# Performance work log

Measured on AMD Instinct MI355X. Metric: run time of the kernel, lower is better.

The kernel has to match this reference:

```python
import jax, jax.numpy as jnp
import numpy as np

N_NODES = 50000
N_EDGES = 800000
IN_CH = 128
OUT_CH = 64
SELF_LOOP_W = 2.0  # improved=True in GCNConv


def setup_inputs() -> dict:
    key = jax.random.key(0)
    k1, k2, k3, k4 = jax.random.split(key, 4)
    x = jax.random.normal(k1, (N_NODES, IN_CH), dtype=jnp.float32)
    edge_index = jax.random.randint(k2, (2, N_EDGES), 0, N_NODES, dtype=jnp.int64)
    edge_weight = jax.random.uniform(k3, (N_EDGES,), dtype=jnp.float32)
    W = jax.random.normal(k4, (IN_CH, OUT_CH), dtype=jnp.float32) / np.sqrt(IN_CH)
    b = jnp.zeros((OUT_CH,), dtype=jnp.float32)
    return {"x": x, "edge_index": edge_index, "edge_weight": edge_weight, "W": W, "b": b}


def reference(x, edge_index, edge_weight, W, b):
    # Only the first GCNConv layer runs (the torch loop returns after k=0).
    N = x.shape[0]
    row, col = edge_index[0], edge_index[1]  # source, target

    # gcn_norm with add_self_loops=True, improved=True (fill value 2.0)
    loop_idx = jnp.arange(N, dtype=edge_index.dtype)
    row_f = jnp.concatenate([row, loop_idx])
    col_f = jnp.concatenate([col, loop_idx])
    ew_f = jnp.concatenate([edge_weight, jnp.full((N,), SELF_LOOP_W, dtype=edge_weight.dtype)])

    deg = jax.ops.segment_sum(ew_f, col_f, num_segments=N)          # [N]
    dinv = jnp.where(deg > 0, jax.lax.rsqrt(deg), 0.0)
    norm = dinv[row_f] * ew_f * dinv[col_f]                          # [E+N]

    # linear transform then normalized sparse aggregation
    xw = x @ W                                                       # [N, out]
    msg = norm[:, None] * xw[row_f]                                  # [E+N, out] gather
    out = jax.ops.segment_sum(msg, col_f, num_segments=N)           # [N, out] scatter-add
    return out + b
```

## Files before the change

### kernel.cpp

```cpp
#include <hip/hip_runtime.h>

constexpr int N    = 50000;
constexpr int E    = 800000;
constexpr int CIN  = 128;
constexpr int COUT = 64;
constexpr float SELF_LOOP_W = 2.0f;

constexpr int NB   = (N + 63) / 64;
constexpr int CAP  = 1536;
constexpr int EPB  = 2048;
constexpr int PBLK = (E + EPB - 1) / EPB;

typedef float          vfloat4  __attribute__((ext_vector_type(4)));
typedef int            vint2    __attribute__((ext_vector_type(2)));
typedef int            vint4    __attribute__((ext_vector_type(4)));
typedef unsigned short vushort4 __attribute__((ext_vector_type(4)));

__device__ __forceinline__ unsigned short f2bf(float f) {
    unsigned int u = __float_as_uint(f);
    u += 0x7FFFu + ((u >> 16) & 1u);
    return (unsigned short)(u >> 16);
}
__device__ __forceinline__ float bf2f(unsigned short h) {
    return __uint_as_float(((unsigned int)h) << 16);
}

__global__ __launch_bounds__(512) void partition_kernel(const int* __restrict__ row,
                                                        const int* __restrict__ col,
                                                        const float* __restrict__ ew,
                                                        int* __restrict__ bcur,
                                                        float* __restrict__ deg,
                                                        vint2* __restrict__ pk) {
    __shared__ int lhist[NB];
    __shared__ int lbase[NB];
    const int t  = threadIdx.x;
    const int e  = blockIdx.x * EPB + t * 4;
    const bool valid = (e < E);

    for (int i = t; i < NB; i += 512) lhist[i] = 0;
    __syncthreads();

    vint4   c4;
    vfloat4 w4;
    if (valid) {
        c4 = *(const vint4*)(col + e);
        w4 = *(const vfloat4*)(ew + e);
        #pragma unroll
        for (int u = 0; u < 4; ++u) {
            atomicAdd(&lhist[c4[u] >> 6], 1);
            atomicAdd(&deg[c4[u]], w4[u]);
        }
    }
    __syncthreads();

    for (int i = t; i < NB; i += 512) {
        int h = lhist[i];
        if (h > 0) lbase[i] = i * CAP + atomicAdd(&bcur[i], h);
    }
    __syncthreads();

    if (valid) {
        vint4 r4 = *(const vint4*)(row + e);
        #pragma unroll
        for (int u = 0; u < 4; ++u) {
            int c   = c4[u];
            int bkt = c >> 6;
            int p   = atomicAdd(&lbase[bkt], 1);
            if (p < (bkt + 1) * CAP) {
                vint2 v;
                v.x = r4[u] | ((c & 63) << 20);
                v.y = __float_as_int(w4[u]);
                pk[p] = v;
            }
        }
    }
}

__global__ __launch_bounds__(256) void xw_kernel(const float* __restrict__ x,
                                                 const float* __restrict__ W,
                                                 const float* __restrict__ deg,
                                                 unsigned short* __restrict__ xwh,
                                                 float* __restrict__ dinv) {
    __shared__ __align__(16) float xs[64][132];

    const int t    = threadIdx.x;
    const int b    = blockIdx.x;
    const int base = b * 64;

    #pragma unroll
    for (int i = 0; i < 8; ++i) {
        int f4  = i * 256 + t;
        int r   = f4 >> 5;
        int c4  = f4 & 31;
        int node = base + r;
        if (node >= N) node = N - 1;
        *(vfloat4*)&xs[r][c4 * 4] = *(const vfloat4*)(x + (size_t)node * CIN + c4 * 4);
    }
    __syncthreads();

    if (t < 64) {
        int node = base + t;
        if (node < N) dinv[node] = rsqrtf(SELF_LOOP_W + deg[node]);
    }

    const int tc = t & 15;
    const int tn = t >> 4;

    float acc[4][4];
    #pragma unroll
    for (int i = 0; i < 4; ++i)
        #pragma unroll
        for (int j = 0; j < 4; ++j) acc[i][j] = 0.f;

    const float* Wp = W + tc * 4;
    #pragma unroll 4
    for (int k = 0; k < CIN; k += 4) {
        vfloat4 b0 = *(const vfloat4*)(Wp + (size_t)(k + 0) * COUT);
        vfloat4 b1 = *(const vfloat4*)(Wp + (size_t)(k + 1) * COUT);
        vfloat4 b2 = *(const vfloat4*)(Wp + (size_t)(k + 2) * COUT);
        vfloat4 b3 = *(const vfloat4*)(Wp + (size_t)(k + 3) * COUT);
        #pragma unroll
        for (int i = 0; i < 4; ++i) {
            vfloat4 a = *(const vfloat4*)&xs[tn * 4 + i][k];
            #pragma unroll
            for (int j = 0; j < 4; ++j)
                acc[i][j] += a[0] * b0[j] + a[1] * b1[j] + a[2] * b2[j] + a[3] * b3[j];
        }
    }

    #pragma unroll
    for (int i = 0; i < 4; ++i) {
        int node = base + tn * 4 + i;
        if (node >= N) continue;
        vushort4 hv;
        #pragma unroll
        for (int j = 0; j < 4; ++j) hv[j] = f2bf(acc[i][j]);
        *(vushort4*)(xwh + (size_t)node * COUT + tc * 4) = hv;
    }
}

__global__ __launch_bounds__(512) void aggregate_kernel(const int* __restrict__ bcur,
                                                        const vint2* __restrict__ pk,
                                                        const float* __restrict__ dinv,
                                                        const unsigned short* __restrict__ xwh,
                                                        const float* __restrict__ bias,
                                                        float* __restrict__ out) {
    __shared__ int   rawx[CAP];
    __shared__ float rawn[CAP];
    __shared__ int   s_r[CAP];
    __shared__ float s_n[CAP];
    __shared__ int   lhist[64], lofs[64], lcur[64];

    const int t    = threadIdx.x;
    const int lane = t & 63;
    const int wv   = t >> 6;
    const int b    = blockIdx.x;
    const int base = b * CAP;
    const int cnt  = min(bcur[b], CAP);

    if (t < 64) lhist[t] = 0;
    __syncthreads();

    for (int j = t; j < cnt; j += 512) {
        vint2 v = pk[base + j];
        rawx[j] = v.x;
        rawn[j] = __int_as_float(v.y) * dinv[v.x & 0xFFFFF];
        atomicAdd(&lhist[(v.x >> 20) & 63], 1);
    }
    __syncthreads();

    if (t < 64) {
        int v = lhist[t];
        int s = v;
        #pragma unroll
        for (int d = 1; d < 64; d <<= 1) {
            int u = __shfl_up(s, d);
            if (lane >= d) s += u;
        }
        lofs[t] = s - v;
        lcur[t] = s - v;
    }
    __syncthreads();

    for (int j = t; j < cnt; j += 512) {
        int xv = rawx[j];
        int p  = atomicAdd(&lcur[(xv >> 20) & 63], 1);
        s_r[p] = xv & 0xFFFFF;
        s_n[p] = rawn[j];
    }
    __syncthreads();

    const int q  = lane >> 4;
    const int c4 = lane & 15;

    for (int nd = wv; nd < 64; nd += 8) {
        int node = b * 64 + nd;
        if (node >= N) continue;
        int s0 = lofs[nd];
        int e0 = s0 + lhist[nd];

        float a0 = 0.f, a1 = 0.f, a2 = 0.f, a3 = 0.f;
        for (int i = s0; i < e0; i += 16) {
            int rr[4]; float nn[4]; vushort4 vv[4];
            #pragma unroll
            for (int u = 0; u < 4; ++u) {
                int j = i + 4 * u + q;
                bool ok = (j < e0);
                rr[u] = ok ? s_r[j] : s_r[s0];
                nn[u] = ok ? s_n[j] : 0.f;
            }
            #pragma unroll
            for (int u = 0; u < 4; ++u)
                vv[u] = *(const vushort4*)(xwh + (size_t)rr[u] * COUT + c4 * 4);
            #pragma unroll
            for (int u = 0; u < 4; ++u) {
                a0 += nn[u] * bf2f(vv[u][0]);
                a1 += nn[u] * bf2f(vv[u][1]);
                a2 += nn[u] * bf2f(vv[u][2]);
                a3 += nn[u] * bf2f(vv[u][3]);
            }
        }
        a0 += __shfl_xor(a0, 16); a0 += __shfl_xor(a0, 32);
        a1 += __shfl_xor(a1, 16); a1 += __shfl_xor(a1, 32);
        a2 += __shfl_xor(a2, 16); a2 += __shfl_xor(a2, 32);
        a3 += __shfl_xor(a3, 16); a3 += __shfl_xor(a3, 32);

        if (q == 0) {
            float dc = dinv[node];
            float s2 = SELF_LOOP_W * dc * dc;
            vushort4 sh = *(const vushort4*)(xwh + (size_t)node * COUT + c4 * 4);
            vfloat4  bv = *(const vfloat4*)(bias + c4 * 4);
            vfloat4  o;
            o[0] = dc * a0 + s2 * bf2f(sh[0]) + bv[0];
            o[1] = dc * a1 + s2 * bf2f(sh[1]) + bv[1];
            o[2] = dc * a2 + s2 * bf2f(sh[2]) + bv[2];
            o[3] = dc * a3 + s2 * bf2f(sh[3]) + bv[3];
            *(vfloat4*)(out + (size_t)node * COUT + c4 * 4) = o;
        }
    }
}

extern "C" void kernel_launch(void* const* d_in, const int* in_sizes, int n_in,
                              void* d_out, int out_size, void* d_ws, size_t ws_size,
                              hipStream_t stream) {
    const float* x  = (const float*)d_in[0];
    const int*   ei = (const int*)d_in[1];
    const float* ew = (const float*)d_in[2];
    const float* W  = (const float*)d_in[3];
    const float* b  = (const float*)d_in[4];
    float* out = (float*)d_out;

    unsigned short* xwh  = (unsigned short*)d_ws;
    float*          dinv = (float*)(xwh + (size_t)N * COUT);
    float*          deg  = dinv + N;
    int*            bcur = (int*)(deg + N);
    vint2*          pk   = (vint2*)(bcur + NB + 2);

    const int* rowp = ei;
    const int* colp = ei + E;

    hipMemsetAsync(deg, 0, (size_t)(N + NB + 2) * sizeof(int), stream);
    partition_kernel<<<PBLK, 512, 0, stream>>>(rowp, colp, ew, bcur, deg, pk);
    xw_kernel       <<<NB, 256, 0, stream>>>(x, W, deg, xwh, dinv);
    aggregate_kernel<<<NB, 512, 0, stream>>>(bcur, pk, dinv, xwh, b, out);
}
```

Baseline: 180.2 us.

## Replace block-local histogram partitioning with per-edge global atomics on sub-buckets

The partition kernel drops its shared-memory histogram, the two block barriers and the per-block base reservation. Each edge now claims a slot directly with a global atomic on one of four sub-bucket counters per destination bucket, chosen by thread index to spread contention. The aggregate kernel gathers the four sub-buckets into a contiguous shared buffer. This trades barrier and shared-atomic overhead for roughly 800K global atomics on the counters. It also caps each sub-bucket at 384 entries, so a skewed split across sub-buckets can overflow one and drop edges.

```diff
diff --git a/kernel.cpp b/kernel.cpp
--- a/kernel.cpp
+++ b/kernel.cpp
@@ -6,10 +6,10 @@
 constexpr int COUT = 64;
 constexpr float SELF_LOOP_W = 2.0f;
 
-constexpr int NB   = (N + 63) / 64;
-constexpr int CAP  = 1536;
-constexpr int EPB  = 2048;
-constexpr int PBLK = (E + EPB - 1) / EPB;
+constexpr int NB     = (N + 63) / 64;
+constexpr int SUBCAP = 384;
+constexpr int CAP    = 4 * SUBCAP;
+constexpr int PBLK   = (E + 1023) / 1024;
 
 typedef float          vfloat4  __attribute__((ext_vector_type(4)));
 typedef int            vint2    __attribute__((ext_vector_type(2)));
@@ -25,54 +25,33 @@
     return __uint_as_float(((unsigned int)h) << 16);
 }
 
-__global__ __launch_bounds__(512) void partition_kernel(const int* __restrict__ row,
+__global__ __launch_bounds__(256) void partition_kernel(const int* __restrict__ row,
                                                         const int* __restrict__ col,
                                                         const float* __restrict__ ew,
                                                         int* __restrict__ bcur,
                                                         float* __restrict__ deg,
                                                         vint2* __restrict__ pk) {
-    __shared__ int lhist[NB];
-    __shared__ int lbase[NB];
-    const int t  = threadIdx.x;
-    const int e  = blockIdx.x * EPB + t * 4;
-    const bool valid = (e < E);
-
-    for (int i = t; i < NB; i += 512) lhist[i] = 0;
-    __syncthreads();
-
-    vint4   c4;
-    vfloat4 w4;
-    if (valid) {
-        c4 = *(const vint4*)(col + e);
-        w4 = *(const vfloat4*)(ew + e);
-        #pragma unroll
-        for (int u = 0; u < 4; ++u) {
-            atomicAdd(&lhist[c4[u] >> 6], 1);
-            atomicAdd(&deg[c4[u]], w4[u]);
-        }
-    }
-    __syncthreads();
-
-    for (int i = t; i < NB; i += 512) {
-        int h = lhist[i];
-        if (h > 0) lbase[i] = i * CAP + atomicAdd(&bcur[i], h);
-    }
-    __syncthreads();
-
-    if (valid) {
-        vint4 r4 = *(const vint4*)(row + e);
-        #pragma unroll
-        for (int u = 0; u < 4; ++u) {
-            int c   = c4[u];
-            int bkt = c >> 6;
-            int p   = atomicAdd(&lbase[bkt], 1);
-            if (p < (bkt + 1) * CAP) {
-                vint2 v;
-                v.x = r4[u] | ((c & 63) << 20);
-                v.y = __float_as_int(w4[u]);
-                pk[p] = v;
-            }
-        }
+    const int t = blockIdx.x * 256 + threadIdx.x;
+    const int e = t * 4;
+    if (e >= E) return;
+
+    vint4   c4 = *(const vint4*)(col + e);
+    vint4   r4 = *(const vint4*)(row + e);
+    vfloat4 w4 = *(const vfloat4*)(ew + e);
+
+    #pragma unroll
+    for (int u = 0; u < 4; ++u) {
+        int c   = c4[u];
+        int bkt = c >> 6;
+        int sub = (threadIdx.x + u) & 3;
+        int p   = atomicAdd(&bcur[bkt * 4 + sub], 1);
+        if (p < SUBCAP) {
+            vint2 v;
+            v.x = r4[u] | ((c & 63) << 20);
+            v.y = __float_as_int(w4[u]);
+            pk[(size_t)bkt * CAP + sub * SUBCAP + p] = v;
+        }
+        atomicAdd(&deg[c], w4[u]);
     }
 }
 
@@ -155,18 +134,24 @@
     const int lane = t & 63;
     const int wv   = t >> 6;
     const int b    = blockIdx.x;
-    const int base = b * CAP;
-    const int cnt  = min(bcur[b], CAP);
+    const size_t base = (size_t)b * CAP;
 
     if (t < 64) lhist[t] = 0;
     __syncthreads();
 
-    for (int j = t; j < cnt; j += 512) {
-        vint2 v = pk[base + j];
-        rawx[j] = v.x;
-        rawn[j] = __int_as_float(v.y) * dinv[v.x & 0xFFFFF];
-        atomicAdd(&lhist[(v.x >> 20) & 63], 1);
-    }
+    int ofs = 0;
+    #pragma unroll
+    for (int s = 0; s < 4; ++s) {
+        int cs = min(bcur[b * 4 + s], SUBCAP);
+        for (int j = t; j < cs; j += 512) {
+            vint2 v = pk[base + s * SUBCAP + j];
+            rawx[ofs + j] = v.x;
+            rawn[ofs + j] = __int_as_float(v.y) * dinv[v.x & 0xFFFFF];
+            atomicAdd(&lhist[(v.x >> 20) & 63], 1);
+        }
+        ofs += cs;
+    }
+    const int cnt = ofs;
     __syncthreads();
 
     if (t < 64) {
@@ -254,13 +239,13 @@
     float*          dinv = (float*)(xwh + (size_t)N * COUT);
     float*          deg  = dinv + N;
     int*            bcur = (int*)(deg + N);
-    vint2*          pk   = (vint2*)(bcur + NB + 2);
+    vint2*          pk   = (vint2*)(bcur + NB * 4);
 
     const int* rowp = ei;
     const int* colp = ei + E;
 
-    hipMemsetAsync(deg, 0, (size_t)(N + NB + 2) * sizeof(int), stream);
-    partition_kernel<<<PBLK, 512, 0, stream>>>(rowp, colp, ew, bcur, deg, pk);
+    hipMemsetAsync(deg, 0, (size_t)(N + NB * 4) * sizeof(int), stream);
+    partition_kernel<<<PBLK, 256, 0, stream>>>(rowp, colp, ew, bcur, deg, pk);
     xw_kernel       <<<NB, 256, 0, stream>>>(x, W, deg, xwh, dinv);
     aggregate_kernel<<<NB, 512, 0, stream>>>(bcur, pk, dinv, xwh, b, out);
 }
```

Result: slower. 240.2 us (+33.3%).
